# Optimization experiments

Hardware: AMD Instinct MI355X
Metric: run time of the kernel (lower is better)

## Reference

```python
import jax, jax.numpy as jnp
import numpy as np

GLOBAL = 3
BETA = 10
CR, CO, CS = 9, 2, 1
N_PCA = 45
PARENTS = [0, 1, 2, 0, 4, 5, 0, 7, 8, 0, 10, 11, 0, 13, 14]
JOINT_REORDER_MESH = {4: 743, 8: 333, 12: 443, 16: 555, 20: 678}


def rodrigues(r):
    # r: [..., 3] axis-angle -> [..., 3, 3] rotation matrix
    theta = jnp.sqrt(jnp.sum(r * r, axis=-1, keepdims=True) + 1e-8)
    n = r / theta
    th = theta[..., None]
    c, s = jnp.cos(th), jnp.sin(th)
    nx, ny, nz = n[..., 0], n[..., 1], n[..., 2]
    z = jnp.zeros_like(nx)
    K = jnp.stack([z, -nz, ny, nz, z, -nx, -ny, nx, z], axis=-1).reshape(r.shape[:-1] + (3, 3))
    outer = n[..., :, None] * n[..., None, :]
    eye = jnp.eye(3, dtype=r.dtype)
    return c * eye + (1.0 - c) * outer + s * K


def setup_inputs() -> dict:
    key = jax.random.key(0)
    ks = jax.random.split(key, 12)
    B, T, D = 32, 128, 5376
    out_dim = N_PCA + GLOBAL + BETA + CR + CO + CS  # 70
    return {
        "x": jax.random.normal(ks[0], (B, T, D), dtype=jnp.float32),
        "W": jax.random.normal(ks[1], (out_dim, D), dtype=jnp.float32) * 0.01,
        "b": jax.random.normal(ks[2], (out_dim,), dtype=jnp.float32) * 0.01,
        "hand_ppal_comps": jax.random.normal(ks[3], (N_PCA, 45), dtype=jnp.float32) * 0.1,
        "mean_hand": jax.random.normal(ks[4], (45,), dtype=jnp.float32) * 0.1,
        "hand_template": jax.random.normal(ks[5], (778, 3), dtype=jnp.float32) * 0.05,
        "shapedirs": jax.random.normal(ks[6], (778, 3, 10), dtype=jnp.float32) * 0.01,
        "posedirs": jax.random.normal(ks[7], (778, 3, 135), dtype=jnp.float32) * 0.01,
        "J_reg": jax.random.uniform(ks[8], (16, 778), dtype=jnp.float32) / 778.0,
        "lbs_weights": jax.nn.softmax(jax.random.normal(ks[9], (778, 16), dtype=jnp.float32), axis=-1),
    }


def _forward(x, W, b, hand_ppal_comps, mean_hand, hand_template, shapedirs, posedirs, J_reg, lbs_weights):
    N, T, _ = x.shape
    params = x @ W.T + b  # [N,T,70]
    n_pca = hand_ppal_comps.shape[0]
    off = GLOBAL + n_pca
    theta = params[..., :off]
    beta = params[..., off:off + BETA]
    c_r = params[..., off + BETA:off + BETA + CR]
    c_o = params[..., off + BETA + CR:off + BETA + CR + CO]
    c_s = params[..., off + BETA + CR + CO:off + BETA + CR + CO + CS]

    # pose from PCA
    hand_posed = theta[..., GLOBAL:] @ hand_ppal_comps + mean_hand  # [N,T,45]
    hand_posed = jnp.concatenate([theta[..., :GLOBAL], hand_posed], axis=-1)  # [N,T,48]

    # shape blendshapes and joints
    hand_shaped = jnp.einsum('vck,btk->btvc', shapedirs, beta) + hand_template  # [N,T,778,3]
    J = jnp.einsum('jv,btvc->btjc', J_reg, hand_shaped)  # [N,T,16,3]

    # pose blendshapes (lrotmin: flattened Rodrigues matrices of the 15 finger joints)
    rod135 = rodrigues(hand_posed[..., GLOBAL:].reshape(N, T, 15, 3)).reshape(N, T, 135)
    curr_hand = hand_shaped + jnp.einsum('vck,btk->btvc', posedirs, rod135)

    # global rigid transformation (kinematic tree)
    rot16 = rodrigues(hand_posed.reshape(N, T, 16, 3))  # [N,T,16,3,3]
    row = jnp.broadcast_to(jnp.array([0.0, 0.0, 0.0, 1.0], dtype=x.dtype), (N, T, 1, 4))
    T0 = jnp.concatenate([jnp.concatenate([rot16[:, :, 0], J[:, :, 0, :, None]], axis=-1), row], axis=-2)  # [N,T,4,4]
    parents = np.array(PARENTS)
    rel = (J[:, :, 1:] - J[:, :, parents])[..., None]  # [N,T,15,3,1]
    op = jnp.concatenate([rot16[:, :, 1:], rel], axis=-1)  # [N,T,15,3,4]
    row15 = jnp.broadcast_to(jnp.array([0.0, 0.0, 0.0, 1.0], dtype=x.dtype), (N, T, 15, 1, 4))
    op = jnp.concatenate([op, row15], axis=-2)  # [N,T,15,4,4]
    res = [T0]
    for i in range(15):
        res.append(res[PARENTS[i]] @ op[:, :, i])
    results = jnp.stack(res, axis=2)  # [N,T,16,4,4]

    ext_J = jnp.concatenate([J, jnp.zeros((N, T, 16, 1), dtype=x.dtype)], axis=-1)
    corr = jnp.einsum('btjik,btjk->btji', results, ext_J)  # [N,T,16,4]
    A = results - jnp.concatenate([jnp.zeros((N, T, 16, 4, 3), dtype=x.dtype), corr[..., None]], axis=-1)
    J3d = results[..., :3, 3]  # [N,T,16,3]

    # linear blend skinning
    Tv = jnp.einsum('btjik,vj->btvik', A, lbs_weights)  # [N,T,778,4,4]
    curr_h = jnp.concatenate([curr_hand, jnp.ones((N, T, 778, 1), dtype=x.dtype)], axis=-1)
    mesh = jnp.einsum('btvij,btvj->btvi', Tv, curr_h)[..., :3]  # [N,T,778,3]

    jr = lambda i: J3d[:, :, i]
    mv = lambda v: mesh[:, :, v]
    J3d_re = jnp.stack([jr(0), jr(13), jr(14), jr(15), mv(743), jr(1), jr(2), jr(3), mv(333),
                        jr(4), jr(5), jr(6), mv(443), jr(10), jr(11), jr(12), mv(555),
                        jr(7), jr(8), jr(9), mv(678)], axis=2)  # [N,T,21,3]

    c_r3 = c_r.reshape(N, T, 3, 3)
    J2d = (J3d_re @ c_r3)[..., :2]
    J2d = c_s[:, :, None] * J2d + c_o[:, :, None]
    return (J2d, theta, beta)


def reference(x, W, b, hand_ppal_comps, mean_hand, hand_template, shapedirs, posedirs, J_reg, lbs_weights):
    return _forward(x, W, b, hand_ppal_comps, mean_hand, hand_template, shapedirs, posedirs, J_reg, lbs_weights)
```

## Files before the change

### kernel.cpp

```cpp
#include <hip/hip_runtime.h>
#include <hip/hip_bf16.h>

typedef short short8 __attribute__((ext_vector_type(8)));
typedef float float4_ __attribute__((ext_vector_type(4)));
typedef unsigned short ushort_t;

#define OUT_THETA 172032
#define OUT_BETA  368640
#define NROW 4096
#define KDIM 5376
#define NPAD 80
#define KS 14
#define KCH 12
#define LDS_STRIDE 392

__device__ __constant__ int c_jslot[16] = {0,5,6,7,9,10,11,17,18,19,13,14,15,1,2,3};
__device__ __constant__ int c_vslot[5]  = {4,8,12,16,20};

__device__ inline short f2bf(float f) {
  union { float f; unsigned u; } v; v.f = f;
  unsigned r = v.u + 0x7fffu + ((v.u >> 16) & 1u);
  return (short)(r >> 16);
}

__device__ inline short8 cvt8(float4_ a, float4_ b) {
  short8 r;
  r[0]=f2bf(a[0]); r[1]=f2bf(a[1]); r[2]=f2bf(a[2]); r[3]=f2bf(a[3]);
  r[4]=f2bf(b[0]); r[5]=f2bf(b[1]); r[6]=f2bf(b[2]); r[7]=f2bf(b[3]);
  return r;
}

__global__ __launch_bounds__(256) void setup_kernel(
    const float* __restrict__ W, const float* __restrict__ shapedirs,
    const float* __restrict__ posedirs, const float* __restrict__ Jreg,
    const float* __restrict__ tmpl, const float* __restrict__ lbs,
    ushort_t* __restrict__ wfrag, float* __restrict__ jsd, float* __restrict__ jt,
    float* __restrict__ psel, float* __restrict__ ssel, float* __restrict__ tsel,
    float* __restrict__ wsel)
{
  int b = blockIdx.x, t = threadIdx.x;
  if (b < 210) {
    int idx = b*256 + t;
    int n = idx / 672, kg = idx % 672;
    short8 o;
    if (n < 70) {
      const float* wp = W + (size_t)n*KDIM + kg*8;
      float4_ w0 = *(const float4_*)wp;
      float4_ w1 = *(const float4_*)(wp+4);
      o = cvt8(w0, w1);
    } else {
      o = (short8){0,0,0,0,0,0,0,0};
    }
    *(short8*)(wfrag + ((size_t)kg*NPAD + n)*8) = o;
  } else if (b < 342) {
    int wv = (b-210)*4 + (t>>6);
    int l = t & 63;
    float p = 0.f;
    if (wv < 480) {
      int j = wv/30, r = wv%30, c = r/10, kk = r%10;
      for (int v = l; v < 778; v += 64) p += Jreg[j*778+v]*shapedirs[(v*3+c)*10+kk];
    } else {
      int o = wv-480; int j = o/3, c = o%3;
      for (int v = l; v < 778; v += 64) p += Jreg[j*778+v]*tmpl[v*3+c];
    }
    for (int off = 32; off > 0; off >>= 1) p += __shfl_down(p, off);
    if (l == 0) { if (wv < 480) jsd[wv] = p; else jt[wv-480] = p; }
  } else {
    const int vtx[5] = {743,333,443,555,678};
    for (int s = t; s < 2270; s += 256) {
      if (s < 2025) { int vi = s/405, r = s%405, c = r/135, kk = r%135;
        psel[s] = posedirs[((size_t)vtx[vi]*3 + c)*135 + kk]; }
      else if (s < 2175) { int u = s-2025; int vi = u/30, r = u%30, c = r/10, kk = r%10;
        ssel[u] = shapedirs[((size_t)vtx[vi]*3 + c)*10 + kk]; }
      else if (s < 2190) { int u = s-2175; int vi = u/3, c = u%3;
        tsel[u] = tmpl[vtx[vi]*3 + c]; }
      else if (s < 2270) { int u = s-2190; int vi = u/16, j = u%16;
        wsel[u] = lbs[vtx[vi]*16 + j]; }
    }
  }
}

__global__ __launch_bounds__(256) void gemm_params(
    const float* __restrict__ x, const ushort_t* __restrict__ wfrag,
    float* __restrict__ part)
{
  __shared__ ushort_t As[64*LDS_STRIDE];
  int t = threadIdx.x;
  int rb = blockIdx.x & 63;
  int kq = blockIdx.x >> 6;
  int m_base = rb << 6;
  int k0 = kq * (KCH*32);

  #pragma unroll
  for (int h = 0; h < 2; ++h) {
    float4_ u0[6], u1[6];
    int dst[6];
    #pragma unroll
    for (int j = 0; j < 6; ++j) {
      int flat = (h*6 + j)*256 + t;
      int row = flat / 48, g = flat - row*48;
      const float* p = x + (size_t)(m_base + row)*KDIM + k0 + g*8;
      u0[j] = *(const float4_*)p;
      u1[j] = *(const float4_*)(p + 4);
      dst[j] = row*LDS_STRIDE + g*8;
    }
    #pragma unroll
    for (int j = 0; j < 6; ++j)
      *(short8*)&As[dst[j]] = cvt8(u0[j], u1[j]);
  }
  __syncthreads();

  int l = t & 63, w = t >> 6;
  int q = l >> 4, lm = l & 15;
  const ushort_t* bp = wfrag + ((size_t)((k0>>3) + q)*NPAD + lm)*8;
  const ushort_t* arow = &As[(w*16 + lm)*LDS_STRIDE + q*8];

  float4_ acc0 = {0.f,0.f,0.f,0.f}, acc1 = acc0, acc2 = acc0, acc3 = acc0, acc4 = acc0;

  short8 bb[2][5];
  #pragma unroll
  for (int s = 0; s < 2; ++s) {
    #pragma unroll
    for (int n = 0; n < 5; ++n)
      bb[s][n] = *(const short8*)(bp + (size_t)s*(4*NPAD*8) + n*128);
  }

  #pragma unroll
  for (int c = 0; c < KCH; ++c) {
    const int sb = c & 1;
    short8 af = *(const short8*)(arow + c*32);
    acc0 = __builtin_amdgcn_mfma_f32_16x16x32_bf16(af, bb[sb][0], acc0, 0, 0, 0);
    acc1 = __builtin_amdgcn_mfma_f32_16x16x32_bf16(af, bb[sb][1], acc1, 0, 0, 0);
    acc2 = __builtin_amdgcn_mfma_f32_16x16x32_bf16(af, bb[sb][2], acc2, 0, 0, 0);
    acc3 = __builtin_amdgcn_mfma_f32_16x16x32_bf16(af, bb[sb][3], acc3, 0, 0, 0);
    acc4 = __builtin_amdgcn_mfma_f32_16x16x32_bf16(af, bb[sb][4], acc4, 0, 0, 0);
    if (c + 2 < KCH) {
      #pragma unroll
      for (int n = 0; n < 5; ++n)
        bb[sb][n] = *(const short8*)(bp + (size_t)(c+2)*(4*NPAD*8) + n*128);
    }
  }

  int m0 = m_base + w*16;
  float* op = part + ((size_t)kq*NROW + m0 + q*4)*NPAD + lm;
  #pragma unroll
  for (int r = 0; r < 4; ++r) {
    op[(size_t)r*NPAD +  0] = acc0[r];
    op[(size_t)r*NPAD + 16] = acc1[r];
    op[(size_t)r*NPAD + 32] = acc2[r];
    op[(size_t)r*NPAD + 48] = acc3[r];
    op[(size_t)r*NPAD + 64] = acc4[r];
  }
}

__global__ __launch_bounds__(64) void decode_kernel(
    const float* __restrict__ part, const float* __restrict__ bvec,
    const float* __restrict__ comps, const float* __restrict__ meanh,
    const float* __restrict__ jsd, const float* __restrict__ jt,
    const float* __restrict__ psel, const float* __restrict__ ssel,
    const float* __restrict__ tsel, const float* __restrict__ wsel,
    float* __restrict__ out)
{
  int row = blockIdx.x;
  int l = threadIdx.x;
  __shared__ float P[70];
  __shared__ float HP[48];
  __shared__ float R[16][9];
  __shared__ float Jl[48];
  __shared__ float RES[16][16];
  __shared__ float Al[16][16];
  __shared__ float CH[5][4];
  __shared__ float M3[21][3];

  {
    float v = bvec[l];
    #pragma unroll
    for (int k = 0; k < KS; ++k) v += part[((size_t)k*NROW + row)*NPAD + l];
    P[l] = v;
    if (l < 48) out[OUT_THETA + (size_t)row*48 + l] = v;
    else if (l < 58) out[OUT_BETA + (size_t)row*10 + (l-48)] = v;
    if (l < 6) {
      int c2 = l + 64;
      float w = bvec[c2];
      #pragma unroll
      for (int k = 0; k < KS; ++k) w += part[((size_t)k*NROW + row)*NPAD + c2];
      P[c2] = w;
    }
  }
  __syncthreads();

  if (l < 45) {
    float s = meanh[l];
    for (int k = 0; k < 45; ++k) s += P[3+k]*comps[k*45 + l];
    HP[3+l] = s;
  } else if (l < 48) HP[l-45] = P[l-45];
  __syncthreads();

  if (l < 16) {
    float rx = HP[3*l], ry = HP[3*l+1], rz = HP[3*l+2];
    float th = sqrtf(rx*rx + ry*ry + rz*rz + 1e-8f);
    float inv = 1.0f/th;
    float nx = rx*inv, ny = ry*inv, nz = rz*inv;
    float cth = cosf(th), sth = sinf(th), mc = 1.0f - cth;
    R[l][0] = cth + mc*nx*nx;     R[l][1] = mc*nx*ny - sth*nz;  R[l][2] = mc*nx*nz + sth*ny;
    R[l][3] = mc*ny*nx + sth*nz;  R[l][4] = cth + mc*ny*ny;     R[l][5] = mc*ny*nz - sth*nx;
    R[l][6] = mc*nz*nx - sth*ny;  R[l][7] = mc*nz*ny + sth*nx;  R[l][8] = cth + mc*nz*nz;
  }
  if (l < 48) {
    float s = jt[l];
    #pragma unroll
    for (int k = 0; k < 10; ++k) s += jsd[l*10+k]*P[48+k];
    Jl[l] = s;
  }
  __syncthreads();

  if (l < 16) {
    int r = l >> 2, c = l & 3;
    RES[0][l] = (r < 3) ? ((c < 3) ? R[0][3*r+c] : Jl[r]) : ((c == 3) ? 1.f : 0.f);
  }
  __syncthreads();
  constexpr int PARS[15] = {0,1,2,0,4,5,0,7,8,0,10,11,0,13,14};
  #pragma unroll
  for (int i = 0; i < 15; ++i) {
    const int p = PARS[i];
    if (l < 16) {
      int r = l >> 2, c = l & 3;
      float s = (c == 3) ? RES[p][4*r+3] : 0.f;
      #pragma unroll
      for (int k = 0; k < 3; ++k) {
        float opv = (c < 3) ? R[i+1][3*k+c] : (Jl[3*(i+1)+k] - Jl[3*p+k]);
        s += RES[p][4*r+k]*opv;
      }
      RES[i+1][l] = s;
    }
    __syncthreads();
  }

  {
    int j = l >> 2, r = l & 3;
    float corr = RES[j][4*r]*Jl[3*j] + RES[j][4*r+1]*Jl[3*j+1] + RES[j][4*r+2]*Jl[3*j+2];
    Al[j][4*r+0] = RES[j][4*r+0];
    Al[j][4*r+1] = RES[j][4*r+1];
    Al[j][4*r+2] = RES[j][4*r+2];
    Al[j][4*r+3] = RES[j][4*r+3] - corr;
  }
  if (l < 15) {
    int vi = l/3, ci = l%3;
    float s = tsel[l];
    #pragma unroll
    for (int k = 0; k < 10; ++k) s += ssel[l*10+k]*P[48+k];
    for (int j15 = 0; j15 < 15; ++j15) {
      #pragma unroll
      for (int e = 0; e < 9; ++e) s += psel[l*135 + j15*9 + e]*R[j15+1][e];
    }
    CH[vi][ci] = s;
  }
  __syncthreads();

  if (l < 48) {
    int j = l/3, c = l%3;
    M3[c_jslot[j]][c] = RES[j][4*c+3];
  } else if (l < 63) {
    int s0 = l - 48; int vi = s0/3, r = s0%3;
    float m = 0.f;
    #pragma unroll
    for (int j = 0; j < 16; ++j) {
      float tv = Al[j][4*r]*CH[vi][0] + Al[j][4*r+1]*CH[vi][1]
               + Al[j][4*r+2]*CH[vi][2] + Al[j][4*r+3];
      m += wsel[vi*16+j]*tv;
    }
    M3[c_vslot[vi]][r] = m;
  }
  __syncthreads();

  if (l < 42) {
    int k = l >> 1, d = l & 1;
    float s = M3[k][0]*P[58 + d] + M3[k][1]*P[58 + 3 + d] + M3[k][2]*P[58 + 6 + d];
    out[((size_t)row*21 + k)*2 + d] = P[69]*s + P[67+d];
  }
}

extern "C" void kernel_launch(void* const* d_in, const int* in_sizes, int n_in,
                              void* d_out, int out_size, void* d_ws, size_t ws_size,
                              hipStream_t stream) {
  const float* x         = (const float*)d_in[0];
  const float* W         = (const float*)d_in[1];
  const float* bvec      = (const float*)d_in[2];
  const float* comps     = (const float*)d_in[3];
  const float* meanh     = (const float*)d_in[4];
  const float* tmpl      = (const float*)d_in[5];
  const float* shapedirs = (const float*)d_in[6];
  const float* posedirs  = (const float*)d_in[7];
  const float* Jreg      = (const float*)d_in[8];
  const float* lbs       = (const float*)d_in[9];

  const size_t PART_ONE = (size_t)NROW*NPAD*4;

  char* ws = (char*)d_ws;
  float*    part  = (float*)ws;
  ushort_t* wfrag = (ushort_t*)(ws + (size_t)KS*PART_ONE);
  char*     tb    = ws + (size_t)KS*PART_ONE + 860160;
  float* jsd  = (float*)tb;
  float* jt   = (float*)(tb + 1920);
  float* psel = (float*)(tb + 1920 + 192);
  float* ssel = (float*)(tb + 1920 + 192 + 8100);
  float* tsel = (float*)(tb + 1920 + 192 + 8100 + 600);
  float* wsel = (float*)(tb + 1920 + 192 + 8100 + 600 + 60);
  float* out  = (float*)d_out;

  hipLaunchKernelGGL(setup_kernel, dim3(343), dim3(256), 0, stream,
                     W, shapedirs, posedirs, Jreg, tmpl, lbs,
                     wfrag, jsd, jt, psel, ssel, tsel, wsel);
  hipLaunchKernelGGL(gemm_params, dim3(64*KS), dim3(256), 0, stream,
                     x, wfrag, part);
  hipLaunchKernelGGL(decode_kernel, dim3(4096), dim3(64), 0, stream,
                     part, bvec, comps, meanh, jsd, jt, psel, ssel, tsel, wsel, out);
}
```

Measured before the change: 184.0 us.

## Load x tiles directly into LDS as fp32 with swizzle, convert at MFMA time

```diff
diff --git a/kernel.cpp b/kernel.cpp
--- a/kernel.cpp
+++ b/kernel.cpp
@@ -10,9 +10,8 @@
 #define NROW 4096
 #define KDIM 5376
 #define NPAD 80
-#define KS 14
-#define KCH 12
-#define LDS_STRIDE 392
+#define KS 21
+#define BK 128
 
 __device__ __constant__ int c_jslot[16] = {0,5,6,7,9,10,11,17,18,19,13,14,15,1,2,3};
 __device__ __constant__ int c_vslot[5]  = {4,8,12,16,20};
@@ -84,72 +83,65 @@
     const float* __restrict__ x, const ushort_t* __restrict__ wfrag,
     float* __restrict__ part)
 {
-  __shared__ ushort_t As[64*LDS_STRIDE];
+  __shared__ float As[64*BK];
   int t = threadIdx.x;
   int rb = blockIdx.x & 63;
   int kq = blockIdx.x >> 6;
   int m_base = rb << 6;
-  int k0 = kq * (KCH*32);
-
-  #pragma unroll
-  for (int h = 0; h < 2; ++h) {
-    float4_ u0[6], u1[6];
-    int dst[6];
-    #pragma unroll
-    for (int j = 0; j < 6; ++j) {
-      int flat = (h*6 + j)*256 + t;
-      int row = flat / 48, g = flat - row*48;
-      const float* p = x + (size_t)(m_base + row)*KDIM + k0 + g*8;
-      u0[j] = *(const float4_*)p;
-      u1[j] = *(const float4_*)(p + 4);
-      dst[j] = row*LDS_STRIDE + g*8;
-    }
-    #pragma unroll
-    for (int j = 0; j < 6; ++j)
-      *(short8*)&As[dst[j]] = cvt8(u0[j], u1[j]);
-  }
-  __syncthreads();
+  int k0 = kq * 256;
 
   int l = t & 63, w = t >> 6;
   int q = l >> 4, lm = l & 15;
-  const ushort_t* bp = wfrag + ((size_t)((k0>>3) + q)*NPAD + lm)*8;
-  const ushort_t* arow = &As[(w*16 + lm)*LDS_STRIDE + q*8];
+  int r = w*16 + lm;
+  int sw = r & 7;
 
   float4_ acc0 = {0.f,0.f,0.f,0.f}, acc1 = acc0, acc2 = acc0, acc3 = acc0, acc4 = acc0;
-
-  short8 bb[2][5];
+  const float4_* As4 = (const float4_*)As;
+
   #pragma unroll
-  for (int s = 0; s < 2; ++s) {
-    #pragma unroll
-    for (int n = 0; n < 5; ++n)
-      bb[s][n] = *(const short8*)(bp + (size_t)s*(4*NPAD*8) + n*128);
-  }
-
+  for (int it = 0; it < 2; ++it) {
+    #pragma unroll
+    for (int j = 0; j < 8; ++j) {
+      int f = j*256 + t;
+      int row = f >> 5, p = f & 31;
+      int g = p ^ (row & 7);
+      const float* src = x + (size_t)(m_base + row)*KDIM + k0 + it*BK + g*4;
+      __builtin_amdgcn_global_load_lds(
+          (const __attribute__((address_space(1))) void*)src,
+          (__attribute__((address_space(3))) void*)&As[(size_t)f*4], 16, 0, 0);
+    }
+    __syncthreads();
+
+    #pragma unroll
+    for (int c = 0; c < 4; ++c) {
+      int cc = it*4 + c;
+      int Lg = c*8 + q*2;
+      float4_ f0 = As4[r*32 + (Lg ^ sw)];
+      float4_ f1 = As4[r*32 + ((Lg+1) ^ sw)];
+      const ushort_t* bp = wfrag + ((size_t)((k0>>3) + cc*4 + q)*NPAD + lm)*8;
+      short8 b0 = *(const short8*)(bp);
+      short8 b1 = *(const short8*)(bp+128);
+      short8 b2 = *(const short8*)(bp+256);
+      short8 b3 = *(const short8*)(bp+384);
+      short8 b4 = *(const short8*)(bp+512);
+      short8 af = cvt8(f0, f1);
+      acc0 = __builtin_amdgcn_mfma_f32_16x16x32_bf16(af, b0, acc0, 0, 0, 0);
+      acc1 = __builtin_amdgcn_mfma_f32_16x16x32_bf16(af, b1, acc1, 0, 0, 0);
+      acc2 = __builtin_amdgcn_mfma_f32_16x16x32_bf16(af, b2, acc2, 0, 0, 0);
+      acc3 = __builtin_amdgcn_mfma_f32_16x16x32_bf16(af, b3, acc3, 0, 0, 0);
+      acc4 = __builtin_amdgcn_mfma_f32_16x16x32_bf16(af, b4, acc4, 0, 0, 0);
+    }
+    __syncthreads();
+  }
+
+  float* op = part + ((size_t)kq*NROW + m_base + w*16 + q*4)*NPAD + lm;
   #pragma unroll
-  for (int c = 0; c < KCH; ++c) {
-    const int sb = c & 1;
-    short8 af = *(const short8*)(arow + c*32);
-    acc0 = __builtin_amdgcn_mfma_f32_16x16x32_bf16(af, bb[sb][0], acc0, 0, 0, 0);
-    acc1 = __builtin_amdgcn_mfma_f32_16x16x32_bf16(af, bb[sb][1], acc1, 0, 0, 0);
-    acc2 = __builtin_amdgcn_mfma_f32_16x16x32_bf16(af, bb[sb][2], acc2, 0, 0, 0);
-    acc3 = __builtin_amdgcn_mfma_f32_16x16x32_bf16(af, bb[sb][3], acc3, 0, 0, 0);
-    acc4 = __builtin_amdgcn_mfma_f32_16x16x32_bf16(af, bb[sb][4], acc4, 0, 0, 0);
-    if (c + 2 < KCH) {
-      #pragma unroll
-      for (int n = 0; n < 5; ++n)
-        bb[sb][n] = *(const short8*)(bp + (size_t)(c+2)*(4*NPAD*8) + n*128);
-    }
-  }
-
-  int m0 = m_base + w*16;
-  float* op = part + ((size_t)kq*NROW + m0 + q*4)*NPAD + lm;
-  #pragma unroll
-  for (int r = 0; r < 4; ++r) {
-    op[(size_t)r*NPAD +  0] = acc0[r];
-    op[(size_t)r*NPAD + 16] = acc1[r];
-    op[(size_t)r*NPAD + 32] = acc2[r];
-    op[(size_t)r*NPAD + 48] = acc3[r];
-    op[(size_t)r*NPAD + 64] = acc4[r];
+  for (int rr = 0; rr < 4; ++rr) {
+    op[(size_t)rr*NPAD +  0] = acc0[rr];
+    op[(size_t)rr*NPAD + 16] = acc1[rr];
+    op[(size_t)rr*NPAD + 32] = acc2[rr];
+    op[(size_t)rr*NPAD + 48] = acc3[rr];
+    op[(size_t)rr*NPAD + 64] = acc4[rr];
   }
 }
 
```

Result: no change. 183.3 us (-0.4%).
